# Performance work log

Hardware: AMD Instinct MI355X
Metric: run time of the kernel (lower is better)

The kernel has to match this reference:

```python
import jax, jax.numpy as jnp
import numpy as np

N_NODES = 8000
N_EDGES = 64000
HEADS = 8
OUT_C = 512
NEG_SLOPE = 0.2
EPS = 1e-16


def setup_inputs() -> dict:
    key = jax.random.key(0)
    ks = jax.random.split(key, 8)
    x = jax.random.normal(ks[0], (N_NODES, 128), dtype=jnp.float32)
    edge_index = jax.random.randint(ks[1], (2, N_EDGES), 0, N_NODES, dtype=jnp.int64)
    W_gat = jax.random.normal(ks[2], (128, HEADS * OUT_C), dtype=jnp.float32) * 0.05
    b_gat = jax.random.normal(ks[3], (HEADS * OUT_C,), dtype=jnp.float32) * 0.05
    att_src = jax.random.normal(ks[4], (HEADS, OUT_C), dtype=jnp.float32) * 0.05
    att_dst = jax.random.normal(ks[5], (HEADS, OUT_C), dtype=jnp.float32) * 0.05
    W_lin = jax.random.normal(ks[6], (HEADS * OUT_C, 512), dtype=jnp.float32) * 0.02
    b_lin = jax.random.normal(ks[7], (512,), dtype=jnp.float32) * 0.02
    return {"x": x, "edge_index": edge_index, "W_gat": W_gat, "b_gat": b_gat,
            "att_src": att_src, "att_dst": att_dst, "W_lin": W_lin, "b_lin": b_lin}


def reference(x, edge_index, W_gat, b_gat, att_src, att_dst, W_lin, b_lin):
    N = x.shape[0]
    # shared linear projection (PyG GATConv single-tensor input): [N, H, C]
    h = (x @ W_gat).reshape(N, HEADS, OUT_C)
    # add self loops (PyG default add_self_loops=True)
    loop = jnp.arange(N, dtype=edge_index.dtype)
    src = jnp.concatenate([edge_index[0], loop])  # source j
    dst = jnp.concatenate([edge_index[1], loop])  # destination i
    # per-node attention logits: [N, H]
    a_src = jnp.einsum('nhc,hc->nh', h, att_src)
    a_dst = jnp.einsum('nhc,hc->nh', h, att_dst)
    # edge logits, leaky relu
    e = jax.nn.leaky_relu(a_src[src] + a_dst[dst], NEG_SLOPE)  # [E, H]
    # softmax over edges sharing a destination
    emax = jax.ops.segment_max(e, dst, num_segments=N)
    ez = jnp.exp(e - emax[dst])
    denom = jax.ops.segment_sum(ez, dst, num_segments=N)
    alpha = ez / (denom[dst] + EPS)  # [E, H]
    # weighted scatter-add of source features
    msg = h[src] * alpha[:, :, None]  # [E, H, C]
    agg = jax.ops.segment_sum(msg, dst, num_segments=N)  # [N, H, C]
    gat_out = agg.reshape(N, HEADS * OUT_C) + b_gat
    return gat_out @ W_lin + b_lin
```

## Files before the change

### kernel.cpp

```cpp
#include <hip/hip_runtime.h>
#include <hip/hip_bf16.h>

#define NN   8000
#define NE   64000
#define NE2  72000
#define NH   8
#define OC   512
#define HC   4096
#define KIN  128
#define NOUT 512
#define YW   1024
#define MAXDEG 64
#define NEG_SLOPE 0.2f

#define VSRC_NB   128
#define PHA_NB    129

#define PB_GEMM_NB 64
#define FILL_BASE  64
#define BEFF_BASE  346
#define ATT_BASE   362
#define PHB_NB     862

using bf16 = __hip_bfloat16;
typedef float  f32x4  __attribute__((ext_vector_type(4)));
typedef __bf16 bf16x8 __attribute__((ext_vector_type(8)));

static __device__ __forceinline__ void gld_lds16(const bf16* g, bf16* l){
    __builtin_amdgcn_global_load_lds(
        (const __attribute__((address_space(1))) unsigned int*)g,
        (__attribute__((address_space(3))) unsigned int*)l, 16, 0, 0);
}

struct Acc24 { f32x4 a[2][4]; };

static __device__ __forceinline__ void gemm64x128(
    const bf16* __restrict__ A, int lda, const bf16* __restrict__ BT, int ldb,
    int K, bf16* sA, bf16* sB, int tid, Acc24& acc)
{
    const int lane = tid & 63;
    const int w    = tid >> 6;
    const int wm   = w >> 1, wn = w & 1;
    const int m16  = lane & 15, q = lane >> 4;
    const int rA = tid >> 2,  kA = (tid & 3) * 8;
    const int cB0 = tid, cB1 = 256 + tid;
    const int rB0 = cB0 >> 2, kB0 = (cB0 & 3) * 8;
    const int rB1 = cB1 >> 2, kB1 = (cB1 & 3) * 8;
    const size_t gA  = (size_t)rA  * lda + kA;
    const size_t gB0 = (size_t)rB0 * ldb + kB0;
    const size_t gB1 = (size_t)rB1 * ldb + kB1;

    #pragma unroll
    for (int i=0;i<2;++i)
        #pragma unroll
        for (int j=0;j<4;++j)
            #pragma unroll
            for (int r=0;r<4;++r) acc.a[i][j][r] = 0.f;

    gld_lds16(A  + gA,  sA + tid*8);
    gld_lds16(BT + gB0, sB + cB0*8);
    gld_lds16(BT + gB1, sB + cB1*8);
    __syncthreads();

    const int nIter = K / 32;
    for (int it = 0; it < nIter; ++it){
        const int cur = it & 1, nxt = cur ^ 1;
        bf16x8 af[2], bfr[4];
        #pragma unroll
        for (int i=0;i<2;++i)
            af[i]  = *(const bf16x8*)(const void*)(sA + cur*64*32 + ((wm*32 + i*16 + m16)*32 + q*8));
        #pragma unroll
        for (int j=0;j<4;++j)
            bfr[j] = *(const bf16x8*)(const void*)(sB + cur*128*32 + ((wn*64 + j*16 + m16)*32 + q*8));
        if (it + 1 < nIter){
            int ko = (it+1) * 32;
            gld_lds16(A  + gA  + ko, sA + nxt*64*32 + tid*8);
            gld_lds16(BT + gB0 + ko, sB + nxt*128*32 + cB0*8);
            gld_lds16(BT + gB1 + ko, sB + nxt*128*32 + cB1*8);
        }
        #pragma unroll
        for (int i=0;i<2;++i)
            #pragma unroll
            for (int j=0;j<4;++j)
                acc.a[i][j] = __builtin_amdgcn_mfma_f32_16x16x32_bf16(af[i], bfr[j], acc.a[i][j], 0, 0, 0);
        __syncthreads();
    }
}

__global__ __launch_bounds__(256) void k_phaseA(
    const float* __restrict__ W_gat,
    const float* __restrict__ att_src, const float* __restrict__ att_dst,
    bf16* __restrict__ Wg, float* __restrict__ v,
    int* __restrict__ cursors)
{
    const int bid = blockIdx.x;
    const int tid = threadIdx.x;

    if (bid < VSRC_NB){
        int k = bid;
        int lane = tid & 63, g = tid >> 6;
        for (int hh = g; hh < NH; hh += 4){
            const float* wp = W_gat + (size_t)k*HC + hh*OC;
            bf16*        wb = Wg    + (size_t)k*HC + hh*OC;
            const float* as = att_src + hh*OC;
            const float* ad = att_dst + hh*OC;
            float ss = 0.f, sd = 0.f;
            #pragma unroll
            for (int c0=0; c0<OC; c0+=64){
                float wv = wp[c0+lane];
                wb[c0+lane] = __float2bfloat16(wv);
                ss = fmaf(wv, as[c0+lane], ss);
                sd = fmaf(wv, ad[c0+lane], sd);
            }
            #pragma unroll
            for (int off=32; off; off>>=1){
                ss += __shfl_down(ss, off);
                sd += __shfl_down(sd, off);
            }
            if (lane == 0){
                v[k*16 + hh]     = ss;
                v[k*16 + 8 + hh] = sd;
            }
        }
    } else {
        for (int i = tid*4; i < NN; i += 1024){
            int4 z; z.x = z.y = z.z = z.w = 0;
            *reinterpret_cast<int4*>(cursors + i) = z;
        }
    }
}

__global__ __launch_bounds__(256) void k_phaseB(
    const bf16* __restrict__ Wg, const float* __restrict__ W_lin,
    const float* __restrict__ b_gat, const int* __restrict__ eidx,
    bf16* __restrict__ WcT, float* __restrict__ beff_part,
    int* __restrict__ cursors, int* __restrict__ esrc,
    const float* __restrict__ x, const float* __restrict__ v,
    float* __restrict__ a_src, float* __restrict__ a_dst)
{
    __shared__ __align__(16) char smem_raw[16*132*2*4];
    const int bid = blockIdx.x;
    const int tid = threadIdx.x;

    if (bid < PB_GEMM_NB){
        bf16* sA = (bf16*)smem_raw;
        bf16* sB = (bf16*)smem_raw + 64*32;

        const int head = bid >> 3;
        const int rem  = bid & 7;
        const int m0   = (rem >> 2) * 64;
        const int n0   = (rem & 3) * 128;
        const int lane = tid & 63;
        const int w = tid >> 6, wm = w >> 1, wn = w & 1;
        const int m16 = lane & 15, q = lane >> 4;

        const int rA = tid >> 2, kA = (tid & 3) * 8;
        const bf16* Abase = Wg + (size_t)(m0 + rA)*HC + head*OC + kA;

        f32x4 acc[2][4];
        #pragma unroll
        for (int i=0;i<2;++i)
            #pragma unroll
            for (int j=0;j<4;++j)
                #pragma unroll
                for (int r=0;r<4;++r) acc[i][j][r] = 0.f;

        for (int kc = 0; kc < OC; kc += 32){
            __syncthreads();
            gld_lds16(Abase + kc, sA + tid*8);
            #pragma unroll
            for (int u=0; u<4; ++u){
                int idx = tid*4 + u;
                int r    = idx >> 5;
                int gcol = (idx & 31) * 4;
                const float* src = W_lin + (size_t)(head*OC + kc + r)*NOUT + n0 + gcol;
                float4 vv = *(const float4*)src;
                sB[(gcol+0)*32 + r] = __float2bfloat16(vv.x);
                sB[(gcol+1)*32 + r] = __float2bfloat16(vv.y);
                sB[(gcol+2)*32 + r] = __float2bfloat16(vv.z);
                sB[(gcol+3)*32 + r] = __float2bfloat16(vv.w);
            }
            __syncthreads();
            bf16x8 af[2], bfr[4];
            #pragma unroll
            for (int i=0;i<2;++i)
                af[i]  = *(const bf16x8*)(const void*)(sA + ((wm*32 + i*16 + m16)*32 + q*8));
            #pragma unroll
            for (int j=0;j<4;++j)
                bfr[j] = *(const bf16x8*)(const void*)(sB + ((wn*64 + j*16 + m16)*32 + q*8));
            #pragma unroll
            for (int i=0;i<2;++i)
                #pragma unroll
                for (int j=0;j<4;++j)
                    acc[i][j] = __builtin_amdgcn_mfma_f32_16x16x32_bf16(af[i], bfr[j], acc[i][j], 0, 0, 0);
        }

        #pragma unroll
        for (int i=0;i<2;++i){
            int row_base = m0 + wm*32 + i*16 + q*4;
            #pragma unroll
            for (int j=0;j<4;++j){
                int col = n0 + wn*64 + j*16 + m16;
                ushort4 pk;
                bf16 b0 = __float2bfloat16(acc[i][j][0]);
                bf16 b1 = __float2bfloat16(acc[i][j][1]);
                bf16 b2 = __float2bfloat16(acc[i][j][2]);
                bf16 b3 = __float2bfloat16(acc[i][j][3]);
                pk.x = *(unsigned short*)&b0; pk.y = *(unsigned short*)&b1;
                pk.z = *(unsigned short*)&b2; pk.w = *(unsigned short*)&b3;
                *reinterpret_cast<ushort4*>(WcT + (size_t)col*YW + head*KIN + row_base) = pk;
            }
        }
        return;
    }

    if (bid < BEFF_BASE){
        int e = (bid - FILL_BASE)*256 + tid;
        if (e < NE2){
            int src, dst;
            if (e < NE){ src = eidx[e]; dst = eidx[NE+e]; } else { src = dst = e - NE; }
            int pos = atomicAdd(&cursors[dst], 1);
            if (pos < MAXDEG) esrc[dst*MAXDEG + pos] = src;
        }
        return;
    }

    if (bid < ATT_BASE){
        int b = bid - BEFF_BASE;
        int o = tid * 2;
        const float* bg = b_gat + b*256;
        const float* wl = W_lin + (size_t)b*256*NOUT + o;
        float a0 = 0.f, a1 = 0.f;
        #pragma unroll 4
        for (int r=0; r<256; ++r){
            float bv = bg[r];
            float2 wv = *(const float2*)(wl + (size_t)r*NOUT);
            a0 = fmaf(bv, wv.x, a0);
            a1 = fmaf(bv, wv.y, a1);
        }
        beff_part[b*NOUT + o]     = a0;
        beff_part[b*NOUT + o + 1] = a1;
        return;
    }

    float (*xs)[132] = (float(*)[132])smem_raw;
    float (*vt)[132] = (float(*)[132])(smem_raw + 16*132*4);
    int node0 = (bid - ATT_BASE) * 16;
    {
        const float* xg = x + (size_t)node0*KIN;
        int row = tid >> 4, co = (tid & 15) * 8;
        float4 v0 = *(const float4*)(xg + row*KIN + co);
        float4 v1 = *(const float4*)(xg + row*KIN + co + 4);
        *(float4*)&xs[row][co]     = v0;
        *(float4*)&xs[row][co + 4] = v1;
    }
    {
        int base = tid*8;
        #pragma unroll
        for (int j=0;j<8;++j){
            int idx = base + j;
            vt[idx & 15][idx >> 4] = v[idx];
        }
    }
    __syncthreads();
    int ln = tid >> 4, o = tid & 15;
    float acc = 0.f;
    #pragma unroll
    for (int k0=0;k0<KIN;k0+=4){
        float4 xv = *(const float4*)&xs[ln][k0];
        float4 vv = *(const float4*)&vt[o][k0];
        acc += xv.x*vv.x + xv.y*vv.y + xv.z*vv.z + xv.w*vv.w;
    }
    int node = node0 + ln;
    if (o < 8) a_src[node*NH + o]     = acc;
    else       a_dst[node*NH + o - 8] = acc;
}

__global__ __launch_bounds__(256) void k_agg(const int* __restrict__ cnts,
    const int* __restrict__ esrc, const float* __restrict__ a_src,
    const float* __restrict__ a_dst, const float* __restrict__ x,
    bf16* __restrict__ Y)
{
    int node = blockIdx.x*4 + (threadIdx.x >> 6);
    int lane = threadIdx.x & 63;
    int s0 = node*MAXDEG, s1 = s0 + min(cnts[node], MAXDEG);
    int g = lane >> 3, h = lane & 7;
    float adl = a_dst[node*NH + h];
    float m = -1e30f, sum = 0.f;
    for (int e = s0 + g; e < s1; e += 8){
        float l = a_src[esrc[e]*NH + h] + adl;
        l = l > 0.f ? l : NEG_SLOPE*l;
        float mn = fmaxf(m, l);
        sum = sum*__expf(m - mn) + __expf(l - mn);
        m = mn;
    }
    #pragma unroll
    for (int d=8; d<64; d<<=1){
        float mo = __shfl_xor(m, d);
        float so = __shfl_xor(sum, d);
        float mn = fmaxf(m, mo);
        sum = sum*__expf(m - mn) + so*__expf(mo - mn);
        m = mn;
    }
    float inv = 1.f / (sum + 1e-16f);
    float acc[16];
    #pragma unroll
    for (int j=0;j<16;++j) acc[j] = 0.f;

    int src_n = esrc[s0];
    float2 xv_n = *(const float2*)(x + (size_t)src_n*KIN + lane*2);
    float al_n = (lane < 8) ? a_src[src_n*NH + lane] : 0.f;
    for (int s = s0; s < s1; ++s){
        float2 xv = xv_n;
        float al = al_n;
        if (s + 1 < s1){
            int sn = esrc[s+1];
            xv_n = *(const float2*)(x + (size_t)sn*KIN + lane*2);
            al_n = (lane < 8) ? a_src[sn*NH + lane] : 0.f;
        }
        float wl = 0.f;
        if (lane < 8){
            float l = al + adl;
            l = l > 0.f ? l : NEG_SLOPE*l;
            wl = __expf(l - m) * inv;
        }
        #pragma unroll
        for (int hh=0; hh<8; ++hh){
            float wh = __shfl(wl, hh);
            acc[hh*2]   = fmaf(wh, xv.x, acc[hh*2]);
            acc[hh*2+1] = fmaf(wh, xv.y, acc[hh*2+1]);
        }
    }
    bf16* yp = Y + (size_t)node*YW + lane*2;
    #pragma unroll
    for (int hh=0; hh<8; ++hh){
        bf16 b0 = __float2bfloat16(acc[hh*2]);
        bf16 b1 = __float2bfloat16(acc[hh*2+1]);
        ushort2 pk;
        pk.x = *(unsigned short*)&b0;
        pk.y = *(unsigned short*)&b1;
        *reinterpret_cast<ushort2*>(yp + hh*KIN) = pk;
    }
}

__global__ __launch_bounds__(256) void k_gemm64(
    const bf16* __restrict__ A, const bf16* __restrict__ BT,
    const float* __restrict__ beff_part, const float* __restrict__ b_lin,
    float* __restrict__ C)
{
    __shared__ __align__(16) char smem_raw[24576];
    bf16* sA = (bf16*)smem_raw;
    bf16* sB = (bf16*)(smem_raw + 8192);
    const int tid = threadIdx.x;
    int m0 = blockIdx.x * 64;
    int n0 = blockIdx.y * 128;
    Acc24 acc;
    gemm64x128(A + (size_t)m0*YW, YW, BT + (size_t)n0*YW, YW, YW, sA, sB, tid, acc);
    const int lane = tid & 63;
    const int w = tid >> 6, wm = w >> 1, wn = w & 1;
    const int m16 = lane & 15, q = lane >> 4;
    #pragma unroll
    for (int j=0;j<4;++j){
        int col = n0 + wn*64 + j*16 + m16;
        float bval = b_lin[col];
        #pragma unroll
        for (int p=0;p<16;++p) bval += beff_part[p*NOUT + col];
        #pragma unroll
        for (int i=0;i<2;++i){
            int row_base = m0 + wm*32 + i*16 + q*4;
            #pragma unroll
            for (int r=0;r<4;++r)
                C[(size_t)(row_base + r)*NOUT + col] = acc.a[i][j][r] + bval;
        }
    }
}

extern "C" void kernel_launch(void* const* d_in, const int* in_sizes, int n_in,
                              void* d_out, int out_size, void* d_ws, size_t ws_size,
                              hipStream_t stream)
{
    const float* x       = (const float*)d_in[0];
    const int*   eidx    = (const int*)  d_in[1];
    const float* W_gat   = (const float*)d_in[2];
    const float* b_gat   = (const float*)d_in[3];
    const float* att_src = (const float*)d_in[4];
    const float* att_dst = (const float*)d_in[5];
    const float* W_lin   = (const float*)d_in[6];
    const float* b_lin   = (const float*)d_in[7];
    float* out = (float*)d_out;

    char* p = (char*)d_ws;
    auto alloc = [&](size_t bytes){ void* r = (void*)p; p += (bytes + 255) & ~(size_t)255; return r; };
    bf16*  Wg        = (bf16*) alloc((size_t)KIN*HC*2);
    bf16*  WcT       = (bf16*) alloc((size_t)NOUT*YW*2);
    bf16*  Ybuf      = (bf16*) alloc((size_t)NN*YW*2);
    float* v         = (float*)alloc((size_t)KIN*16*4);
    float* a_src     = (float*)alloc((size_t)NN*NH*4);
    float* a_dst     = (float*)alloc((size_t)NN*NH*4);
    int*   esrc      = (int*)  alloc((size_t)NN*MAXDEG*4);
    int*   cursors   = (int*)  alloc((size_t)NN*4);
    float* beff_part = (float*)alloc((size_t)16*NOUT*4);
    if ((size_t)(p - (char*)d_ws) > ws_size) return;

    k_phaseA<<<PHA_NB, 256, 0, stream>>>(W_gat, att_src, att_dst, Wg, v, cursors);
    k_phaseB<<<PHB_NB, 256, 0, stream>>>(Wg, W_lin, b_gat, eidx, WcT, beff_part,
                                         cursors, esrc, x, v, a_src, a_dst);
    k_agg<<<NN/4, 256, 0, stream>>>(cursors, esrc, a_src, a_dst, x, Ybuf);
    k_gemm64<<<dim3(NN/64, NOUT/128), 256, 0, stream>>>(Ybuf, WcT, beff_part, b_lin, out);
}
```

Measured before the change: 139.9 us.

## Use BK=64 swizzled LDS tiles and XCD-aware block remap in final GEMM

Doubles the K-step of the final 8000x512x1024 GEMM from 32 to 64 and stores LDS tiles with an XOR swizzle to avoid bank conflicts on fragment reads. It also switches to a 1D grid of 500 blocks remapped so that consecutive tile ids land on the same XCD, so neighbouring M-rows share the A-tile in L2. This halves barrier count per K and improves L2 locality, but doubles LDS use per block (48KB), which may lower occupancy.

```diff
diff --git a/kernel.cpp b/kernel.cpp
--- a/kernel.cpp
+++ b/kernel.cpp
@@ -22,6 +22,8 @@
 #define ATT_BASE   362
 #define PHB_NB     862
 
+#define GEMM_NB   500
+
 using bf16 = __hip_bfloat16;
 typedef float  f32x4  __attribute__((ext_vector_type(4)));
 typedef __bf16 bf16x8 __attribute__((ext_vector_type(8)));
@@ -34,7 +36,7 @@
 
 struct Acc24 { f32x4 a[2][4]; };
 
-static __device__ __forceinline__ void gemm64x128(
+static __device__ __forceinline__ void gemm64x128_bk64(
     const bf16* __restrict__ A, int lda, const bf16* __restrict__ BT, int ldb,
     int K, bf16* sA, bf16* sB, int tid, Acc24& acc)
 {
@@ -42,13 +44,20 @@
     const int w    = tid >> 6;
     const int wm   = w >> 1, wn = w & 1;
     const int m16  = lane & 15, q = lane >> 4;
-    const int rA = tid >> 2,  kA = (tid & 3) * 8;
-    const int cB0 = tid, cB1 = 256 + tid;
-    const int rB0 = cB0 >> 2, kB0 = (cB0 & 3) * 8;
-    const int rB1 = cB1 >> 2, kB1 = (cB1 & 3) * 8;
-    const size_t gA  = (size_t)rA  * lda + kA;
-    const size_t gB0 = (size_t)rB0 * ldb + kB0;
-    const size_t gB1 = (size_t)rB1 * ldb + kB1;
+
+    const int cA0 = tid,        cA1 = tid + 256;
+    const int rA0 = cA0 >> 3,   jA0 = (cA0 & 7) ^ (rA0 & 7);
+    const int rA1 = cA1 >> 3,   jA1 = (cA1 & 7) ^ (rA1 & 7);
+    const size_t gA0 = (size_t)rA0 * lda + jA0 * 8;
+    const size_t gA1 = (size_t)rA1 * lda + jA1 * 8;
+    size_t gB[4]; int cB[4];
+    #pragma unroll
+    for (int u=0; u<4; ++u){
+        int c = tid + 256*u;
+        int r = c >> 3, j = (c & 7) ^ (r & 7);
+        cB[u] = c;
+        gB[u] = (size_t)r * ldb + j * 8;
+    }
 
     #pragma unroll
     for (int i=0;i<2;++i)
@@ -57,32 +66,45 @@
             #pragma unroll
             for (int r=0;r<4;++r) acc.a[i][j][r] = 0.f;
 
-    gld_lds16(A  + gA,  sA + tid*8);
-    gld_lds16(BT + gB0, sB + cB0*8);
-    gld_lds16(BT + gB1, sB + cB1*8);
+    gld_lds16(A  + gA0, sA + cA0*8);
+    gld_lds16(A  + gA1, sA + cA1*8);
+    #pragma unroll
+    for (int u=0; u<4; ++u) gld_lds16(BT + gB[u], sB + cB[u]*8);
     __syncthreads();
 
-    const int nIter = K / 32;
+    const int nIter = K / 64;
     for (int it = 0; it < nIter; ++it){
         const int cur = it & 1, nxt = cur ^ 1;
-        bf16x8 af[2], bfr[4];
-        #pragma unroll
-        for (int i=0;i<2;++i)
-            af[i]  = *(const bf16x8*)(const void*)(sA + cur*64*32 + ((wm*32 + i*16 + m16)*32 + q*8));
-        #pragma unroll
-        for (int j=0;j<4;++j)
-            bfr[j] = *(const bf16x8*)(const void*)(sB + cur*128*32 + ((wn*64 + j*16 + m16)*32 + q*8));
+        bf16x8 af[2][2], bfr[4][2];
+        #pragma unroll
+        for (int ks=0; ks<2; ++ks){
+            #pragma unroll
+            for (int i=0;i<2;++i){
+                int row = wm*32 + i*16 + m16;
+                int p   = (ks*4 + q) ^ (row & 7);
+                af[i][ks] = *(const bf16x8*)(const void*)(sA + cur*64*64 + row*64 + p*8);
+            }
+            #pragma unroll
+            for (int j=0;j<4;++j){
+                int row = wn*64 + j*16 + m16;
+                int p   = (ks*4 + q) ^ (row & 7);
+                bfr[j][ks] = *(const bf16x8*)(const void*)(sB + cur*128*64 + row*64 + p*8);
+            }
+        }
         if (it + 1 < nIter){
-            int ko = (it+1) * 32;
-            gld_lds16(A  + gA  + ko, sA + nxt*64*32 + tid*8);
-            gld_lds16(BT + gB0 + ko, sB + nxt*128*32 + cB0*8);
-            gld_lds16(BT + gB1 + ko, sB + nxt*128*32 + cB1*8);
-        }
-        #pragma unroll
-        for (int i=0;i<2;++i)
-            #pragma unroll
-            for (int j=0;j<4;++j)
-                acc.a[i][j] = __builtin_amdgcn_mfma_f32_16x16x32_bf16(af[i], bfr[j], acc.a[i][j], 0, 0, 0);
+            const size_t ko = (size_t)(it+1) * 64;
+            gld_lds16(A  + gA0 + ko, sA + nxt*64*64 + cA0*8);
+            gld_lds16(A  + gA1 + ko, sA + nxt*64*64 + cA1*8);
+            #pragma unroll
+            for (int u=0; u<4; ++u) gld_lds16(BT + gB[u] + ko, sB + nxt*128*64 + cB[u]*8);
+        }
+        #pragma unroll
+        for (int ks=0; ks<2; ++ks)
+            #pragma unroll
+            for (int i=0;i<2;++i)
+                #pragma unroll
+                for (int j=0;j<4;++j)
+                    acc.a[i][j] = __builtin_amdgcn_mfma_f32_16x16x32_bf16(af[i][ks], bfr[j][ks], acc.a[i][j], 0, 0, 0);
         __syncthreads();
     }
 }
@@ -348,14 +370,19 @@
     const float* __restrict__ beff_part, const float* __restrict__ b_lin,
     float* __restrict__ C)
 {
-    __shared__ __align__(16) char smem_raw[24576];
-    bf16* sA = (bf16*)smem_raw;
-    bf16* sB = (bf16*)(smem_raw + 8192);
+    __shared__ __align__(16) bf16 sA[2*64*64];
+    __shared__ __align__(16) bf16 sB[2*128*64];
     const int tid = threadIdx.x;
-    int m0 = blockIdx.x * 64;
-    int n0 = blockIdx.y * 128;
+
+    const int orig = blockIdx.x;
+    const int xcd = orig & 7, slot = orig >> 3;
+    const int wgid = (xcd < 4 ? xcd*63 : 252 + (xcd-4)*62) + slot;
+    const int m0 = (wgid >> 2) * 64;
+    const int n0 = (wgid & 3) * 128;
+
     Acc24 acc;
-    gemm64x128(A + (size_t)m0*YW, YW, BT + (size_t)n0*YW, YW, YW, sA, sB, tid, acc);
+    gemm64x128_bk64(A + (size_t)m0*YW, YW, BT + (size_t)n0*YW, YW, YW, sA, sB, tid, acc);
+
     const int lane = tid & 63;
     const int w = tid >> 6, wm = w >> 1, wn = w & 1;
     const int m16 = lane & 15, q = lane >> 4;
@@ -406,5 +433,5 @@
     k_phaseB<<<PHB_NB, 256, 0, stream>>>(Wg, W_lin, b_gat, eidx, WcT, beff_part,
                                          cursors, esrc, x, v, a_src, a_dst);
     k_agg<<<NN/4, 256, 0, stream>>>(cursors, esrc, a_src, a_dst, x, Ybuf);
-    k_gemm64<<<dim3(NN/64, NOUT/128), 256, 0, stream>>>(Ybuf, WcT, beff_part, b_lin, out);
-}
+    k_gemm64<<<GEMM_NB, 256, 0, stream>>>(Ybuf, WcT, beff_part, b_lin, out);
+}
```

New measurement: 136.1 us. -2.7%, faster.
